# Performance work log

Hardware: AMD Instinct MI355X
Metric: run time of the kernel (lower is better)

## Reference

```python
import jax, jax.numpy as jnp
import numpy as np
import math

H = 2048
NH = 16
HD = H // NH  # 128
EPS_LN = 1e-5
RES_SCALE_MAX = 0.3

def _nan_clean(x, lim=10000.0):
    return jnp.nan_to_num(x, nan=0.0, posinf=lim, neginf=-lim)

def setup_inputs() -> dict:
    key = jax.random.key(0)
    ks = jax.random.split(key, 12)
    B, S, T = 4, 2048, 256
    std = 1.0 / math.sqrt(H)
    return {
        "hidden_states": jax.random.normal(ks[0], (B, S, H), jnp.float32),
        "audio_tokens": jax.random.normal(ks[1], (B, T, H), jnp.float32),
        "attention_mask": jax.random.randint(ks[2], (B, T), 0, 2, jnp.int32),
        "Wq": jax.random.normal(ks[3], (H, H), jnp.float32) * std,
        "bq": jnp.zeros((H,), jnp.float32),
        "Wk": jax.random.normal(ks[4], (H, H), jnp.float32) * std,
        "bk": jnp.zeros((H,), jnp.float32),
        "Wv": jax.random.normal(ks[5], (H, H), jnp.float32) * std,
        "bv": jnp.zeros((H,), jnp.float32),
        "Wo": jax.random.normal(ks[6], (H, H), jnp.float32) * std,
        "bo": jnp.zeros((H,), jnp.float32),
        "ln_gamma": jnp.ones((H,), jnp.float32),
        "ln_beta": jnp.zeros((H,), jnp.float32),
        "residual_scale": jnp.float32(0.05),
    }

def reference(hidden_states, audio_tokens, attention_mask,
              Wq, bq, Wk, bk, Wv, bv, Wo, bo, ln_gamma, ln_beta, residual_scale):
    B, S, _ = hidden_states.shape
    T = audio_tokens.shape[1]
    hs = _nan_clean(hidden_states).astype(jnp.float32)
    at = _nan_clean(audio_tokens).astype(jnp.float32)
    # Q/K/V projections -> (B, heads, len, head_dim)
    def proj(x, W, b, L):
        y = x @ W.T + b
        return y.reshape(B, L, NH, HD).transpose(0, 2, 1, 3)
    q = _nan_clean(proj(hs, Wq, bq, S))
    k = _nan_clean(proj(at, Wk, bk, T))
    v = _nan_clean(proj(at, Wv, bv, T))
    scale = max(math.sqrt(HD), 1e-8)
    scores = jnp.einsum('bhsd,bhtd->bhst', q, k) / scale
    scores = jnp.clip(scores, -50.0, 50.0)
    scores = jnp.nan_to_num(scores, nan=0.0, posinf=50.0, neginf=-50.0)
    # mask: int 0/1 -> attend where > 0.5, broadcast (B,1,1,T)
    attend = (attention_mask.astype(jnp.float32) > 0.5)[:, None, None, :]
    scores = jnp.where(attend, scores, -10000.0)
    scores = jnp.clip(scores, -50.0, 50.0)
    probs = jax.nn.softmax(scores, axis=-1)
    probs = jnp.nan_to_num(probs, nan=0.0, posinf=1.0, neginf=0.0)
    probs = probs / (probs.sum(axis=-1, keepdims=True) + 1e-8)
    # dropout: eval mode -> identity
    ctx = jnp.einsum('bhst,bhtd->bhsd', probs, v)
    ctx = ctx.transpose(0, 2, 1, 3).reshape(B, S, H)
    delta = _nan_clean(ctx @ Wo.T + bo)
    rs = jnp.clip(residual_scale, 0.0, RES_SCALE_MAX)
    delta = rs * delta
    # LayerNorm (biased variance, like torch)
    mu = delta.mean(axis=-1, keepdims=True)
    var = jnp.mean((delta - mu) ** 2, axis=-1, keepdims=True)
    delta = (delta - mu) / jnp.sqrt(var + EPS_LN) * ln_gamma + ln_beta
    return delta
```

## Files before the change

kernel.cpp:

```cpp
#include <hip/hip_runtime.h>
#include <stdint.h>

typedef unsigned short u16;
typedef __attribute__((ext_vector_type(8))) __bf16 bf16x8;
typedef __attribute__((ext_vector_type(4))) float f32x4;

#define AS1 __attribute__((address_space(1)))
#define AS3 __attribute__((address_space(3)))

constexpr int HB = 4;
constexpr int SS = 2048;
constexpr int TT = 256;
constexpr int HH = 2048;
constexpr int NHEAD = 16;
constexpr int HD = 128;

__device__ __forceinline__ u16 f2b(float f) {
  union { float f; uint32_t u; } c; c.f = f;
  return (u16)((c.u + 0x7FFFu + ((c.u >> 16) & 1u)) >> 16);
}

__device__ __forceinline__ float b2f(uint32_t lo16) {
  union { uint32_t u; float f; } c; c.u = lo16 << 16;
  return c.f;
}

__global__ __launch_bounds__(256)
void cast_all(const float* __restrict__ hs, const float* __restrict__ at,
              const float* __restrict__ wq, const float* __restrict__ wk,
              const float* __restrict__ wv, const float* __restrict__ wo,
              u16* __restrict__ o_hs, u16* __restrict__ o_at,
              u16* __restrict__ o_wq, u16* __restrict__ o_wk,
              u16* __restrict__ o_wv, u16* __restrict__ o_wo) {
  const int b = blockIdx.x;
  const float* src; u16* dst; int base;
  if (b < 16384)      { src = hs; dst = o_hs; base = 0; }
  else if (b < 18432) { src = at; dst = o_at; base = 16384; }
  else if (b < 22528) { src = wq; dst = o_wq; base = 18432; }
  else if (b < 26624) { src = wk; dst = o_wk; base = 22528; }
  else if (b < 30720) { src = wv; dst = o_wv; base = 26624; }
  else                { src = wo; dst = o_wo; base = 30720; }
  const size_t i = (size_t)(b - base) * 256 + threadIdx.x;
  const float4 v = *(const float4*)(src + i * 4);
  uint2 pk;
  pk.x = (uint32_t)f2b(v.x) | ((uint32_t)f2b(v.y) << 16);
  pk.y = (uint32_t)f2b(v.z) | ((uint32_t)f2b(v.w) << 16);
  *(uint2*)(dst + i * 4) = pk;
}

template<int MODE>
__global__ __launch_bounds__(512, 2)
void gemm8(const u16* __restrict__ A, const u16* __restrict__ Bw,
           const float* __restrict__ bias, const float* __restrict__ rsp,
           void* __restrict__ outp) {
  constexpr int KD = 2048, NT = 64;
  constexpr int BUF = 16384;
  __shared__ u16 lds[4 * BUF];
  const int tid = threadIdx.x;
  const int wv = tid >> 6, ln = tid & 63;
  const int lq = ln >> 4, lr = ln & 15;
  const int wm = wv >> 2, wn = wv & 3;

  const int linb = blockIdx.y * 8 + blockIdx.x;
  const int ns = (linb & 7) * 32 + (linb >> 3);
  const int m0 = (ns >> 3) * 256;
  const int n0 = (ns & 7) * 256;

  int gOff[2];
#pragma unroll
  for (int c = 0; c < 2; ++c) {
    const int g = c * 512 + tid, sr = g >> 3, s = g & 7, l = s ^ (sr & 7);
    gOff[c] = (2 * sr + (l >> 2)) * KD + (l & 3) * 8;
  }
  const u16* Abase = A + (size_t)m0 * KD;
  const u16* Bbase = Bw + (size_t)n0 * KD;

  int aoff[8], boff[4];
#pragma unroll
  for (int m = 0; m < 8; ++m) {
    const int R = wm * 128 + m * 16 + lr, sr = R >> 1;
    aoff[m] = sr * 64 + ((((R & 1) << 2) + lq) ^ (sr & 7)) * 8;
  }
#pragma unroll
  for (int j = 0; j < 4; ++j) {
    const int R = wn * 64 + j * 16 + lr, sr = R >> 1;
    boff[j] = 8192 + sr * 64 + ((((R & 1) << 2) + lq) ^ (sr & 7)) * 8;
  }

#define STAGE_A(c, k0, buf)                                                      \
  __builtin_amdgcn_global_load_lds((AS1 const void*)(Abase + (k0) + gOff[c]),    \
      (AS3 void*)(lds + (buf) * BUF + ((c) * 512 + wv * 64) * 8), 16, 0, 0)
#define STAGE_B(c, k0, buf)                                                      \
  __builtin_amdgcn_global_load_lds((AS1 const void*)(Bbase + (k0) + gOff[c]),    \
      (AS3 void*)(lds + (buf) * BUF + 8192 + ((c) * 512 + wv * 64) * 8), 16, 0, 0)

  f32x4 acc[8][4];
#pragma unroll
  for (int i = 0; i < 8; ++i)
#pragma unroll
    for (int j = 0; j < 4; ++j) acc[i][j] = (f32x4){0.f, 0.f, 0.f, 0.f};

  STAGE_A(0, 0, 0);  STAGE_A(1, 0, 0);  STAGE_B(0, 0, 0);  STAGE_B(1, 0, 0);
  STAGE_A(0, 32, 1); STAGE_A(1, 32, 1); STAGE_B(0, 32, 1); STAGE_B(1, 32, 1);
  STAGE_A(0, 64, 2); STAGE_A(1, 64, 2); STAGE_B(0, 64, 2); STAGE_B(1, 64, 2);
  asm volatile("s_waitcnt vmcnt(8)" ::: "memory");
  __builtin_amdgcn_s_barrier();
  __builtin_amdgcn_sched_barrier(0);

  bf16x8 af[4], bf[4], afn[4];
#pragma unroll
  for (int j = 0; j < 4; ++j) bf[j] = *(const bf16x8*)(lds + boff[j]);
#pragma unroll
  for (int m = 0; m < 4; ++m) af[m] = *(const bf16x8*)(lds + aoff[m]);
  __builtin_amdgcn_sched_barrier(0);

  for (int t = 0; t < NT; ++t) {
    const u16* bb = lds + (t & 3) * BUF;
    const u16* bn = lds + ((t + 1) & 3) * BUF;
    const int stg = (t + 3) & 3;
    const int k3 = (t + 3) * 32;
    const bool doStage = (t + 3) < NT;

#pragma unroll
    for (int m = 0; m < 4; ++m) afn[m] = *(const bf16x8*)(bb + aoff[4 + m]);
    if (doStage) { STAGE_A(0, k3, stg); STAGE_A(1, k3, stg); }
    asm volatile("s_waitcnt lgkmcnt(4)" ::: "memory");
    __builtin_amdgcn_sched_barrier(0);
    __builtin_amdgcn_s_setprio(1);
#pragma unroll
    for (int m = 0; m < 4; ++m)
#pragma unroll
      for (int j = 0; j < 4; ++j)
        acc[m][j] = __builtin_amdgcn_mfma_f32_16x16x32_bf16(af[m], bf[j], acc[m][j], 0, 0, 0);
    __builtin_amdgcn_s_setprio(0);
    if (doStage) { STAGE_B(0, k3, stg); STAGE_B(1, k3, stg); }
    if (t < NT - 3)       asm volatile("s_waitcnt vmcnt(8)" ::: "memory");
    else if (t == NT - 3) asm volatile("s_waitcnt vmcnt(4)" ::: "memory");
    else                  asm volatile("s_waitcnt vmcnt(0)" ::: "memory");
    asm volatile("s_waitcnt lgkmcnt(0)" ::: "memory");
    __builtin_amdgcn_s_barrier();
    __builtin_amdgcn_sched_barrier(0);
    if (t + 1 < NT) {
#pragma unroll
      for (int m = 0; m < 4; ++m) af[m] = *(const bf16x8*)(bn + aoff[m]);
    }
    __builtin_amdgcn_s_setprio(1);
#pragma unroll
    for (int m = 0; m < 4; ++m)
#pragma unroll
      for (int j = 0; j < 4; ++j)
        acc[4 + m][j] = __builtin_amdgcn_mfma_f32_16x16x32_bf16(afn[m], bf[j], acc[4 + m][j], 0, 0, 0);
    __builtin_amdgcn_s_setprio(0);
    if (t + 1 < NT) {
#pragma unroll
      for (int j = 0; j < 4; ++j) bf[j] = *(const bf16x8*)(bn + boff[j]);
    }
    __builtin_amdgcn_sched_barrier(0);
  }
#undef STAGE_A
#undef STAGE_B

  float bj[4];
#pragma unroll
  for (int j = 0; j < 4; ++j) bj[j] = bias[n0 + wn * 64 + j * 16 + lr];
  float rsv = 0.f;
  if constexpr (MODE == 2 || MODE == 3) rsv = fminf(fmaxf(rsp[0], 0.0f), 0.3f);

#pragma unroll
  for (int i = 0; i < 8; ++i)
#pragma unroll
    for (int j = 0; j < 4; ++j)
#pragma unroll
      for (int r = 0; r < 4; ++r) {
        const int row = m0 + wm * 128 + i * 16 + lq * 4 + r;
        const int col = n0 + wn * 64 + j * 16 + lr;
        const float v = acc[i][j][r] + bj[j];
        if constexpr (MODE == 0) {
          ((u16*)outp)[(size_t)row * 2048 + col] = f2b(v);
        } else if constexpr (MODE == 2) {
          ((float*)outp)[(size_t)row * 2048 + col] = v * rsv;
        } else {
          ((u16*)outp)[(size_t)row * 2048 + col] = f2b(v * rsv);
        }
      }
}

__global__ __launch_bounds__(256, 2)
void gemm_kv(const u16* __restrict__ A, const u16* __restrict__ Wk,
             const u16* __restrict__ Wv, const float* __restrict__ bkp,
             const float* __restrict__ bvp, u16* __restrict__ Ko,
             u16* __restrict__ Vto) {
  constexpr int KD = 2048, NT = 64;
  constexpr int BUFE = 8192;
  __shared__ u16 lds[4 * BUFE];
  const bool isV = blockIdx.z != 0;
  const u16* Bw = isV ? Wv : Wk;
  const float* bias = isV ? bvp : bkp;
  const int tid = threadIdx.x;
  const int wave = tid >> 6, lane = tid & 63;
  const int lq = lane >> 4, lr = lane & 15;
  const int wr = wave >> 1, wc = wave & 1;
  const int m0 = blockIdx.y * 128, n0 = blockIdx.x * 128;

  int gOff[2];
#pragma unroll
  for (int c = 0; c < 2; ++c) {
    const int g = c * 256 + tid, sr = g >> 3, s = g & 7, l = s ^ (sr & 7);
    gOff[c] = (2 * sr + (l >> 2)) * KD + (l & 3) * 8;
  }
  const u16* Abase = A + (size_t)m0 * KD;
  const u16* Bbase = Bw + (size_t)n0 * KD;

  int aoff[4], boff[4];
#pragma unroll
  for (int i = 0; i < 4; ++i) {
    const int R = wr * 64 + i * 16 + lr, sr = R >> 1;
    aoff[i] = sr * 64 + ((((R & 1) << 2) + lq) ^ (sr & 7)) * 8;
  }
#pragma unroll
  for (int j = 0; j < 4; ++j) {
    const int R = wc * 64 + j * 16 + lr, sr = R >> 1;
    boff[j] = 4096 + sr * 64 + ((((R & 1) << 2) + lq) ^ (sr & 7)) * 8;
  }

#define KV_STAGE(t3, buf)                                                         \
  {                                                                               \
    _Pragma("unroll")                                                             \
    for (int c_ = 0; c_ < 2; ++c_) {                                              \
      __builtin_amdgcn_global_load_lds(                                           \
          (AS1 const void*)(Abase + (t3) * 32 + gOff[c_]),                        \
          (AS3 void*)(lds + (buf) * BUFE + (c_ * 256 + wave * 64) * 8), 16, 0, 0);\
      __builtin_amdgcn_global_load_lds(                                           \
          (AS1 const void*)(Bbase + (t3) * 32 + gOff[c_]),                        \
          (AS3 void*)(lds + (buf) * BUFE + 4096 + (c_ * 256 + wave * 64) * 8),    \
          16, 0, 0);                                                              \
    }                                                                             \
  }

  f32x4 acc[4][4];
#pragma unroll
  for (int i = 0; i < 4; ++i)
#pragma unroll
    for (int j = 0; j < 4; ++j) acc[i][j] = (f32x4){0.f, 0.f, 0.f, 0.f};

  KV_STAGE(0, 0); KV_STAGE(1, 1); KV_STAGE(2, 2);
  asm volatile("s_waitcnt vmcnt(8)" ::: "memory");
  __builtin_amdgcn_s_barrier();
  __builtin_amdgcn_sched_barrier(0);

  bf16x8 af[4], bfr[4];
#pragma unroll
  for (int i = 0; i < 4; ++i) af[i] = *(const bf16x8*)(lds + aoff[i]);
#pragma unroll
  for (int j = 0; j < 4; ++j) bfr[j] = *(const bf16x8*)(lds + boff[j]);
  __builtin_amdgcn_sched_barrier(0);

  for (int t = 0; t < NT; ++t) {
    if (t + 3 < NT) KV_STAGE(t + 3, (t + 3) & 3);
    asm volatile("s_waitcnt lgkmcnt(0)" ::: "memory");
    __builtin_amdgcn_sched_barrier(0);
    __builtin_amdgcn_s_setprio(1);
#pragma unroll
    for (int i = 0; i < 4; ++i)
#pragma unroll
      for (int j = 0; j < 4; ++j)
        acc[i][j] = __builtin_amdgcn_mfma_f32_16x16x32_bf16(af[i], bfr[j], acc[i][j], 0, 0, 0);
    __builtin_amdgcn_s_setprio(0);
    if (t < NT - 3)       asm volatile("s_waitcnt vmcnt(8)" ::: "memory");
    else if (t == NT - 3) asm volatile("s_waitcnt vmcnt(4)" ::: "memory");
    else                  asm volatile("s_waitcnt vmcnt(0)" ::: "memory");
    __builtin_amdgcn_s_barrier();
    __builtin_amdgcn_sched_barrier(0);
    if (t + 1 < NT) {
      const u16* bn = lds + ((t + 1) & 3) * BUFE;
#pragma unroll
      for (int i = 0; i < 4; ++i) af[i] = *(const bf16x8*)(bn + aoff[i]);
#pragma unroll
      for (int j = 0; j < 4; ++j) bfr[j] = *(const bf16x8*)(bn + boff[j]);
    }
    __builtin_amdgcn_sched_barrier(0);
  }
#undef KV_STAGE

  float bj[4];
#pragma unroll
  for (int j = 0; j < 4; ++j) bj[j] = bias[n0 + wc * 64 + j * 16 + lr];

#pragma unroll
  for (int i = 0; i < 4; ++i)
#pragma unroll
    for (int j = 0; j < 4; ++j)
#pragma unroll
      for (int r = 0; r < 4; ++r) {
        const int row = m0 + wr * 64 + i * 16 + lq * 4 + r;
        const int col = n0 + wc * 64 + j * 16 + lr;
        const float v = acc[i][j][r] + bj[j];
        if (!isV) {
          Ko[(size_t)row * 2048 + col] = f2b(v);
        } else {
          Vto[(size_t)(row >> 8) * (2048 * 256) + (size_t)col * 256 + (row & 255)] = f2b(v);
        }
      }
}

__global__ __launch_bounds__(512, 2)
void attn_kernel(const u16* __restrict__ Q, const u16* __restrict__ Kb,
                 const u16* __restrict__ Vt, const int* __restrict__ mask,
                 u16* __restrict__ ctx) {
  __shared__ u16 sQ[128 * 128];
  __shared__ u16 sK[2][64 * 128];
  __shared__ u16 sVt[2][128 * 64];
  __shared__ u16 sP[8 * 16 * 72];

  const int tid = threadIdx.x;
  const int wv = tid >> 6, ln = tid & 63;
  const int lq = ln >> 4, lr = ln & 15;
  const int h = blockIdx.y, b = blockIdx.z;
  const int s0blk = blockIdx.x * 128;
  u16* sPw = sP + wv * (16 * 72);

  {
    const size_t qg = ((size_t)b * SS + s0blk) * HH + (size_t)h * HD;
#pragma unroll
    for (int it = 0; it < 4; ++it) {
      const int ub = it * 512 + wv * 64;
      const int u = ub + ln;
      const int row = u >> 4, slot = u & 15, src = slot ^ (row & 15);
      __builtin_amdgcn_global_load_lds((AS1 const void*)(Q + qg + (size_t)row * HH + src * 8),
                                       (AS3 void*)(sQ + (size_t)ub * 8), 16, 0, 0);
    }
  }
#define STAGE_KV(c)                                                                      \
  {                                                                                      \
    const int buf_ = (c) & 1;                                                            \
    _Pragma("unroll")                                                                    \
    for (int it = 0; it < 2; ++it) {                                                     \
      const int ub = it * 512 + wv * 64;                                                 \
      const int u = ub + ln;                                                             \
      const int row = u >> 4, slot = u & 15, src = slot ^ (row & 15);                    \
      const u16* g = Kb + ((size_t)b * TT + (c) * 64 + row) * HH + h * HD + src * 8;     \
      __builtin_amdgcn_global_load_lds((AS1 const void*)g,                               \
          (AS3 void*)(sK[buf_] + (size_t)ub * 8), 16, 0, 0);                             \
    }                                                                                    \
    _Pragma("unroll")                                                                    \
    for (int it = 0; it < 2; ++it) {                                                     \
      const int ub = it * 512 + wv * 64;                                                 \
      const int u = ub + ln;                                                             \
      const int row = u >> 3, slot = u & 7, src = slot ^ (row & 7);                      \
      const u16* g = Vt + ((size_t)b * HH + h * HD + row) * TT + (c) * 64 + src * 8;     \
      __builtin_amdgcn_global_load_lds((AS1 const void*)g,                               \
          (AS3 void*)(sVt[buf_] + (size_t)ub * 8), 16, 0, 0);                            \
    }                                                                                    \
  }
  STAGE_KV(0);
  STAGE_KV(1);

  const float scale = 0.08838834764831845f;
  float m[4] = {-INFINITY, -INFINITY, -INFINITY, -INFINITY};
  float l[4] = {0.f, 0.f, 0.f, 0.f};
  f32x4 o[8];
#pragma unroll
  for (int d0 = 0; d0 < 8; ++d0) o[d0] = (f32x4){0.f, 0.f, 0.f, 0.f};

  const int qrow = wv * 16 + lr;
  const int shsrc = ((lr >> 2) << 4) + lr;

  for (int c = 0; c < 4; ++c) {
    const int buf = c & 1;
    if (c < 3) asm volatile("s_waitcnt vmcnt(4)" ::: "memory");
    else       asm volatile("s_waitcnt vmcnt(0)" ::: "memory");
    __syncthreads();

    bf16x8 qf[4];
#pragma unroll
    for (int kd = 0; kd < 4; ++kd)
      qf[kd] = *(const bf16x8*)(sQ + (size_t)qrow * 128 + (size_t)((kd * 4 + lq) ^ lr) * 8);

    f32x4 sc[4];
#pragma unroll
    for (int tt = 0; tt < 4; ++tt) {
      f32x4 a = (f32x4){0.f, 0.f, 0.f, 0.f};
#pragma unroll
      for (int kd = 0; kd < 4; ++kd) {
        bf16x8 kf = *(const bf16x8*)(sK[buf] + (size_t)(tt * 16 + lr) * 128 + (size_t)((kd * 4 + lq) ^ lr) * 8);
        a = __builtin_amdgcn_mfma_f32_16x16x32_bf16(qf[kd], kf, a, 0, 0, 0);
      }
      sc[tt] = a;
    }

    float lm[4] = {-1e30f, -1e30f, -1e30f, -1e30f};
#pragma unroll
    for (int tt = 0; tt < 4; ++tt) {
      const int att = mask[b * TT + c * 64 + tt * 16 + lr];
#pragma unroll
      for (int r = 0; r < 4; ++r) {
        float v = sc[tt][r] * scale;
        v = fminf(fmaxf(v, -50.f), 50.f);
        v = att ? v : -50.f;
        sc[tt][r] = v;
        lm[r] = fmaxf(lm[r], v);
      }
    }
#pragma unroll
    for (int d = 1; d < 16; d <<= 1)
#pragma unroll
      for (int r = 0; r < 4; ++r) lm[r] = fmaxf(lm[r], __shfl_xor(lm[r], d));

    float alpha[4];
#pragma unroll
    for (int r = 0; r < 4; ++r) {
      const float mn = fmaxf(m[r], lm[r]);
      alpha[r] = __expf(m[r] - mn);
      m[r] = mn;
    }
    float ls[4] = {0.f, 0.f, 0.f, 0.f};
#pragma unroll
    for (int tt = 0; tt < 4; ++tt)
#pragma unroll
      for (int r = 0; r < 4; ++r) {
        const float p = __expf(sc[tt][r] - m[r]);
        sc[tt][r] = p;
        ls[r] += p;
      }
#pragma unroll
    for (int d = 1; d < 16; d <<= 1)
#pragma unroll
      for (int r = 0; r < 4; ++r) ls[r] += __shfl_xor(ls[r], d);
#pragma unroll
    for (int r = 0; r < 4; ++r) l[r] = l[r] * alpha[r] + ls[r];

    const float a0 = __shfl(alpha[0], shsrc), a1 = __shfl(alpha[1], shsrc);
    const float a2 = __shfl(alpha[2], shsrc), a3 = __shfl(alpha[3], shsrc);
    const int rsel = lr & 3;
    const float aq = rsel == 0 ? a0 : rsel == 1 ? a1 : rsel == 2 ? a2 : a3;
    if (!__all(aq >= 1.0f)) {
#pragma unroll
      for (int d0 = 0; d0 < 8; ++d0)
#pragma unroll
        for (int r = 0; r < 4; ++r) o[d0][r] *= aq;
    }

#pragma unroll
    for (int tt = 0; tt < 4; ++tt)
#pragma unroll
      for (int r = 0; r < 4; ++r)
        sPw[(size_t)(lq * 4 + r) * 72 + tt * 16 + lr] = f2b(sc[tt][r]);

    bf16x8 pf[2];
#pragma unroll
    for (int kt = 0; kt < 2; ++kt)
      pf[kt] = *(const bf16x8*)(sPw + (size_t)lr * 72 + kt * 32 + lq * 8);

#pragma unroll
    for (int d0 = 0; d0 < 8; ++d0)
#pragma unroll
      for (int kt = 0; kt < 2; ++kt) {
        bf16x8 vf = *(const bf16x8*)(sVt[buf] + (size_t)(d0 * 16 + lr) * 64 + (size_t)((kt * 4 + lq) ^ (lr & 7)) * 8);
        o[d0] = __builtin_amdgcn_mfma_f32_16x16x32_bf16(vf, pf[kt], o[d0], 0, 0, 0);
      }
    __syncthreads();
    if (c + 2 < 4) STAGE_KV(c + 2);
  }
#undef STAGE_KV

  const float i0 = __shfl(1.0f / l[0], shsrc), i1 = __shfl(1.0f / l[1], shsrc);
  const float i2 = __shfl(1.0f / l[2], shsrc), i3 = __shfl(1.0f / l[3], shsrc);
  const int rsel = lr & 3;
  const float iq = rsel == 0 ? i0 : rsel == 1 ? i1 : rsel == 2 ? i2 : i3;

  const size_t cbase = ((size_t)b * SS + s0blk + wv * 16 + lr) * HH + (size_t)h * HD;
#pragma unroll
  for (int d0 = 0; d0 < 8; ++d0) {
    uint2 w;
    w.x = (uint32_t)f2b(o[d0][0] * iq) | ((uint32_t)f2b(o[d0][1] * iq) << 16);
    w.y = (uint32_t)f2b(o[d0][2] * iq) | ((uint32_t)f2b(o[d0][3] * iq) << 16);
    *(uint2*)(ctx + cbase + d0 * 16 + lq * 4) = w;
  }
}

__global__ __launch_bounds__(256)
void ln_kernel(const u16* __restrict__ in, float* __restrict__ out,
               const float* __restrict__ gamma, const float* __restrict__ beta) {
  const int row = blockIdx.x, tid = threadIdx.x;
  const u16* x = in + (size_t)row * 2048;
  const uint4 raw = *(const uint4*)(x + tid * 8);
  float xv[8];
  xv[0] = b2f(raw.x & 0xFFFFu); xv[1] = b2f(raw.x >> 16);
  xv[2] = b2f(raw.y & 0xFFFFu); xv[3] = b2f(raw.y >> 16);
  xv[4] = b2f(raw.z & 0xFFFFu); xv[5] = b2f(raw.z >> 16);
  xv[6] = b2f(raw.w & 0xFFFFu); xv[7] = b2f(raw.w >> 16);
  float s = 0.f, ss = 0.f;
#pragma unroll
  for (int i = 0; i < 8; ++i) { s += xv[i]; ss += xv[i] * xv[i]; }
#pragma unroll
  for (int d = 1; d < 64; d <<= 1) {
    s += __shfl_xor(s, d);
    ss += __shfl_xor(ss, d);
  }
  __shared__ float rbuf[8];
  const int w = tid >> 6;
  if ((tid & 63) == 0) { rbuf[w] = s; rbuf[4 + w] = ss; }
  __syncthreads();
  s = rbuf[0] + rbuf[1] + rbuf[2] + rbuf[3];
  ss = rbuf[4] + rbuf[5] + rbuf[6] + rbuf[7];
  const float mu = s * (1.0f / 2048.0f);
  const float var = ss * (1.0f / 2048.0f) - mu * mu;
  const float inv = rsqrtf(var + 1e-5f);
  const float4 g0 = *(const float4*)(gamma + tid * 8);
  const float4 g1 = *(const float4*)(gamma + tid * 8 + 4);
  const float4 b0 = *(const float4*)(beta + tid * 8);
  const float4 b1 = *(const float4*)(beta + tid * 8 + 4);
  float4 y0, y1;
  y0.x = (xv[0] - mu) * inv * g0.x + b0.x;
  y0.y = (xv[1] - mu) * inv * g0.y + b0.y;
  y0.z = (xv[2] - mu) * inv * g0.z + b0.z;
  y0.w = (xv[3] - mu) * inv * g0.w + b0.w;
  y1.x = (xv[4] - mu) * inv * g1.x + b1.x;
  y1.y = (xv[5] - mu) * inv * g1.y + b1.y;
  y1.z = (xv[6] - mu) * inv * g1.z + b1.z;
  y1.w = (xv[7] - mu) * inv * g1.w + b1.w;
  float* o = out + (size_t)row * 2048 + tid * 8;
  *(float4*)o = y0;
  *(float4*)(o + 4) = y1;
}

extern "C" void kernel_launch(void* const* d_in, const int* in_sizes, int n_in,
                              void* d_out, int out_size, void* d_ws, size_t ws_size,
                              hipStream_t stream) {
  (void)in_sizes; (void)n_in; (void)out_size; (void)ws_size;
  const float* hs = (const float*)d_in[0];
  const float* at = (const float*)d_in[1];
  const int* mask = (const int*)d_in[2];
  const float* Wq = (const float*)d_in[3];
  const float* bq = (const float*)d_in[4];
  const float* Wk = (const float*)d_in[5];
  const float* bk = (const float*)d_in[6];
  const float* Wv = (const float*)d_in[7];
  const float* bv = (const float*)d_in[8];
  const float* Wo = (const float*)d_in[9];
  const float* bo = (const float*)d_in[10];
  const float* lg = (const float*)d_in[11];
  const float* lb = (const float*)d_in[12];
  const float* rs = (const float*)d_in[13];

  u16* hs_bf = (u16*)d_ws;
  u16* at_bf = hs_bf + 16777216;
  u16* Wq_bf = at_bf + 2097152;
  u16* Wk_bf = Wq_bf + 4194304;
  u16* Wv_bf = Wk_bf + 4194304;
  u16* Wo_bf = Wv_bf + 4194304;
  u16* Q_bf  = Wo_bf + 4194304;
  u16* K_bf  = Q_bf + 16777216;
  u16* Vt_bf = K_bf + 2097152;
  u16* ctx_bf = hs_bf;
  u16* delta_bf = Q_bf;

  cast_all<<<34816, 256, 0, stream>>>(hs, at, Wq, Wk, Wv, Wo,
                                      hs_bf, at_bf, Wq_bf, Wk_bf, Wv_bf, Wo_bf);

  gemm8<0><<<dim3(8, 32), 512, 0, stream>>>(hs_bf, Wq_bf, bq, nullptr, Q_bf);
  gemm_kv<<<dim3(16, 8, 2), 256, 0, stream>>>(at_bf, Wk_bf, Wv_bf, bk, bv, K_bf, Vt_bf);

  attn_kernel<<<dim3(16, 16, 4), 512, 0, stream>>>(Q_bf, K_bf, Vt_bf, mask, ctx_bf);

  gemm8<3><<<dim3(8, 32), 512, 0, stream>>>(ctx_bf, Wo_bf, bo, rs, delta_bf);
  ln_kernel<<<8192, 256, 0, stream>>>(delta_bf, (float*)d_out, lg, lb);
}
```

Before: 266.7 us.

## Load Q fragments straight to registers and swizzle P tile to cut LDS

The attention kernel now reads its Q fragments directly from global memory into registers instead of staging them in a 32KB shared tile. The padded P scratch buffer becomes an XOR-swizzled, unpadded layout, and launch bounds rise to 4 blocks per SM so the smaller LDS footprint can allow more resident blocks. The trailing barrier on the last two KV chunks is also dropped. The tighter launch bound caps registers per thread and may cause spills, and the uncoalesced Q register loads may cost more than the shared-memory staging did.

```diff
diff --git a/kernel.cpp b/kernel.cpp
--- a/kernel.cpp
+++ b/kernel.cpp
@@ -303,33 +303,28 @@
       }
 }
 
-__global__ __launch_bounds__(512, 2)
+__global__ __launch_bounds__(512, 4)
 void attn_kernel(const u16* __restrict__ Q, const u16* __restrict__ Kb,
                  const u16* __restrict__ Vt, const int* __restrict__ mask,
                  u16* __restrict__ ctx) {
-  __shared__ u16 sQ[128 * 128];
   __shared__ u16 sK[2][64 * 128];
   __shared__ u16 sVt[2][128 * 64];
-  __shared__ u16 sP[8 * 16 * 72];
+  __shared__ u16 sP[8 * 16 * 64];
 
   const int tid = threadIdx.x;
   const int wv = tid >> 6, ln = tid & 63;
   const int lq = ln >> 4, lr = ln & 15;
   const int h = blockIdx.y, b = blockIdx.z;
   const int s0blk = blockIdx.x * 128;
-  u16* sPw = sP + wv * (16 * 72);
-
+  u16* sPw = sP + wv * (16 * 64);
+
+  bf16x8 qf[4];
   {
-    const size_t qg = ((size_t)b * SS + s0blk) * HH + (size_t)h * HD;
-#pragma unroll
-    for (int it = 0; it < 4; ++it) {
-      const int ub = it * 512 + wv * 64;
-      const int u = ub + ln;
-      const int row = u >> 4, slot = u & 15, src = slot ^ (row & 15);
-      __builtin_amdgcn_global_load_lds((AS1 const void*)(Q + qg + (size_t)row * HH + src * 8),
-                                       (AS3 void*)(sQ + (size_t)ub * 8), 16, 0, 0);
-    }
-  }
+    const u16* qp = Q + ((size_t)b * SS + s0blk + wv * 16 + lr) * HH + (size_t)h * HD + lq * 8;
+#pragma unroll
+    for (int kd = 0; kd < 4; ++kd) qf[kd] = *(const bf16x8*)(qp + kd * 32);
+  }
+
 #define STAGE_KV(c)                                                                      \
   {                                                                                      \
     const int buf_ = (c) & 1;                                                            \
@@ -362,7 +357,6 @@
 #pragma unroll
   for (int d0 = 0; d0 < 8; ++d0) o[d0] = (f32x4){0.f, 0.f, 0.f, 0.f};
 
-  const int qrow = wv * 16 + lr;
   const int shsrc = ((lr >> 2) << 4) + lr;
 
   for (int c = 0; c < 4; ++c) {
@@ -370,11 +364,6 @@
     if (c < 3) asm volatile("s_waitcnt vmcnt(4)" ::: "memory");
     else       asm volatile("s_waitcnt vmcnt(0)" ::: "memory");
     __syncthreads();
-
-    bf16x8 qf[4];
-#pragma unroll
-    for (int kd = 0; kd < 4; ++kd)
-      qf[kd] = *(const bf16x8*)(sQ + (size_t)qrow * 128 + (size_t)((kd * 4 + lq) ^ lr) * 8);
 
     f32x4 sc[4];
 #pragma unroll
@@ -443,13 +432,18 @@
 #pragma unroll
     for (int tt = 0; tt < 4; ++tt)
 #pragma unroll
-      for (int r = 0; r < 4; ++r)
-        sPw[(size_t)(lq * 4 + r) * 72 + tt * 16 + lr] = f2b(sc[tt][r]);
+      for (int r = 0; r < 4; ++r) {
+        const int q = lq * 4 + r;
+        const int slot = (tt * 2 + (lr >> 3)) ^ ((q >> 1) & 7);
+        sPw[(size_t)q * 64 + slot * 8 + (lr & 7)] = f2b(sc[tt][r]);
+      }
 
     bf16x8 pf[2];
 #pragma unroll
-    for (int kt = 0; kt < 2; ++kt)
-      pf[kt] = *(const bf16x8*)(sPw + (size_t)lr * 72 + kt * 32 + lq * 8);
+    for (int kt = 0; kt < 2; ++kt) {
+      const int slot = (kt * 4 + lq) ^ ((lr >> 1) & 7);
+      pf[kt] = *(const bf16x8*)(sPw + (size_t)lr * 64 + slot * 8);
+    }
 
 #pragma unroll
     for (int d0 = 0; d0 < 8; ++d0)
@@ -458,8 +452,10 @@
         bf16x8 vf = *(const bf16x8*)(sVt[buf] + (size_t)(d0 * 16 + lr) * 64 + (size_t)((kt * 4 + lq) ^ (lr & 7)) * 8);
         o[d0] = __builtin_amdgcn_mfma_f32_16x16x32_bf16(vf, pf[kt], o[d0], 0, 0, 0);
       }
-    __syncthreads();
-    if (c + 2 < 4) STAGE_KV(c + 2);
+    if (c < 2) {
+      __syncthreads();
+      STAGE_KV(c + 2);
+    }
   }
 #undef STAGE_KV
 
```

New measurement: 266.1 us. Within noise of the previous version (-0.2%).
